# Performance work log

Measured on AMD Instinct MI355X. Metric: run time of the kernel, lower is better.

Reference implementation:

```python
import jax, jax.numpy as jnp
import numpy as np

A_, H_, D_, T_, B_ = 12, 6, 192, 80, 8
C_ = 192                      # GATv2 out_channels per head
N_ = B_ * A_                  # sequences
G_ = B_ * T_                  # graphs (one per frame)
E_ = A_ * (A_ - 1)            # 132 directed edges, no self loops
DH_ = D_ // H_


def _ln(x, g, b):
    m = jnp.mean(x, -1, keepdims=True)
    v = jnp.mean((x - m) ** 2, -1, keepdims=True)
    return (x - m) * jax.lax.rsqrt(v + 1e-5) * g + b


def _bn(x, g, b, m, v):  # eval-mode BatchNorm1d over the feature channel
    return (x - m) * jax.lax.rsqrt(v + 1e-5) * g + b


def _forward(state_feat, edge_attr, emb_table, laW1, lab1, bn1g, bn1b, bn1m, bn1v, laW2, lab2, bn2g, bn2b, bn2m, bn2v, laW3, lab3, bn3g, bn3b, bn3m, bn3v, ln1g, ln1b, qkvw, qkvb, outw, outb, ln2g, ln2b, fw1, fb1, fw2, fb2, gwl, gbl, gwr, gbr, gwe, gatt, gbias, ng, nb, padding_mask, agent_ids, edge_index):
    pl = emb_table[jnp.clip(agent_ids, 0)]                                   # [N,12]
    x = jnp.concatenate([state_feat, jnp.broadcast_to(pl[:, None, :], (N_, T_, 12))], -1)
    x = jax.nn.relu(_bn(x @ laW1 + lab1, bn1g, bn1b, bn1m, bn1v))
    x = jax.nn.relu(_bn(x @ laW2 + lab2, bn2g, bn2b, bn2m, bn2v))
    x = jax.nn.relu(_bn(x @ laW3 + lab3, bn3g, bn3b, bn3m, bn3v))
    x_initial = x
    # sinusoidal positional encoding (dropout off / eval)
    pos = jnp.arange(T_, dtype=jnp.float32)[:, None]
    div = jnp.exp(jnp.arange(0, D_, 2, dtype=jnp.float32) * (-np.log(10000.0) / D_))
    pe = jnp.zeros((T_, D_), jnp.float32).at[:, 0::2].set(jnp.sin(pos * div)).at[:, 1::2].set(jnp.cos(pos * div))
    x = x + pe
    causal = jnp.triu(jnp.full((T_, T_), -jnp.inf, jnp.float32), k=1)
    # --- static GAT edge structure (shared by every frame-graph) ---
    src, dst = edge_index[0], edge_index[1]
    onehot = (dst[None, :] == jnp.arange(A_)[:, None]).astype(jnp.float32)   # [A,E]
    cnt = onehot.sum(1)
    ea = edge_attr.reshape(G_, E_, 2)
    # PyG add_self_loops(fill_value='mean'): self-loop attr = mean of incoming-edge attrs
    loop_ea = jnp.einsum('ae,gef->gaf', onehot, ea) / cnt[None, :, None]     # [G,A,2]
    ea2 = jnp.concatenate([ea, loop_ea], axis=1).reshape(-1, 2)              # [G*(E+A),2]
    src2 = jnp.concatenate([src, jnp.arange(A_, dtype=src.dtype)])
    dst2 = jnp.concatenate([dst, jnp.arange(A_, dtype=dst.dtype)])
    off = (jnp.arange(G_, dtype=src.dtype) * A_)[:, None]
    sflat = (src2[None, :] + off).reshape(-1)                                # flattened batch-of-graphs
    dflat = (dst2[None, :] + off).reshape(-1)
    GA = G_ * A_
    for l in range(3):
        # --- causal temporal self-attention (pre-LN, eval: dropout off) ---
        xn = _ln(x, ln1g[l], ln1b[l])
        qkv = xn @ qkvw[l] + qkvb[l]
        q, k, v = jnp.split(qkv, 3, axis=-1)
        q = q.reshape(N_, T_, H_, DH_); k = k.reshape(N_, T_, H_, DH_); v = v.reshape(N_, T_, H_, DH_)
        s = jnp.einsum('nqhd,nkhd->nhqk', q, k) / np.sqrt(DH_) + causal
        s = jnp.where(padding_mask[:, None, None, :], -jnp.inf, s)
        p = jax.nn.softmax(s, axis=-1)
        o = jnp.einsum('nhqk,nkhd->nqhd', p, v).reshape(N_, T_, D_)
        x = x + (o @ outw[l] + outb[l])
        xn = _ln(x, ln2g[l], ln2b[l])
        x = x + (jax.nn.gelu(xn @ fw1[l] + fb1[l], approximate=False) @ fw2[l] + fb2[l])
        # --- framewise GATv2 (concat=False -> mean over heads) ---
        xn = _ln(x, ng[l], nb[l])
        xnodes = xn.reshape(B_, A_, T_, D_).transpose(0, 2, 1, 3).reshape(GA, D_)
        xl = (xnodes @ gwl[l] + gbl[l]).reshape(GA, H_, C_)
        xr = (xnodes @ gwr[l] + gbr[l]).reshape(GA, H_, C_)
        ef = (ea2 @ gwe[l]).reshape(-1, H_, C_)
        xls = xl[sflat]                                                      # gather source features
        msg = jax.nn.leaky_relu(xls + xr[dflat] + ef, 0.2)
        alpha = jnp.einsum('ehc,hc->eh', msg, gatt[l])
        amax = jax.lax.stop_gradient(jax.ops.segment_max(alpha, dflat, num_segments=GA))
        exs = jnp.exp(alpha - amax[dflat])
        den = jax.ops.segment_sum(exs, dflat, num_segments=GA)
        w = exs / den[dflat]                                                 # segment softmax over dst
        agg = jax.ops.segment_sum(w[:, :, None] * xls, dflat, num_segments=GA)
        xg = (agg.mean(axis=1) + gbias[l]).reshape(B_, T_, A_, D_).transpose(0, 2, 1, 3).reshape(N_, T_, D_)
        x = x + xg
    return (x_initial, x)


def setup_inputs():
    ks = iter(jax.random.split(jax.random.key(0), 60))
    def r(shape, s=0.05):
        return jax.random.normal(next(ks), shape, jnp.float32) * s
    pairs = np.array([(i, j) for i in range(A_) for j in range(A_) if i != j], dtype=np.int32)
    return dict(
        state_feat=jax.random.normal(next(ks), (N_, T_, 4), jnp.float32),
        padding_mask=jnp.zeros((N_, T_), bool),
        agent_ids=jax.random.randint(next(ks), (N_,), 0, 600, jnp.int32),
        edge_index=jnp.asarray(pairs.T),
        edge_attr=jax.random.normal(next(ks), (B_, T_, E_, 2), jnp.float32),
        emb_table=r((600, 12), 1.0),
        laW1=r((16, 64)), lab1=jnp.zeros((64,)),
        bn1g=jnp.ones((64,)), bn1b=jnp.zeros((64,)), bn1m=jnp.zeros((64,)), bn1v=jnp.ones((64,)),
        laW2=r((64, 256)), lab2=jnp.zeros((256,)),
        bn2g=jnp.ones((256,)), bn2b=jnp.zeros((256,)), bn2m=jnp.zeros((256,)), bn2v=jnp.ones((256,)),
        laW3=r((256, D_)), lab3=jnp.zeros((D_,)),
        bn3g=jnp.ones((D_,)), bn3b=jnp.zeros((D_,)), bn3m=jnp.zeros((D_,)), bn3v=jnp.ones((D_,)),
        ln1g=jnp.ones((3, D_)), ln1b=jnp.zeros((3, D_)),
        qkvw=r((3, D_, 3 * D_)), qkvb=jnp.zeros((3, 3 * D_)),
        outw=r((3, D_, D_)), outb=jnp.zeros((3, D_)),
        ln2g=jnp.ones((3, D_)), ln2b=jnp.zeros((3, D_)),
        fw1=r((3, D_, 4 * D_)), fb1=jnp.zeros((3, 4 * D_)),
        fw2=r((3, 4 * D_, D_)), fb2=jnp.zeros((3, D_)),
        gwl=r((3, D_, H_ * C_)), gbl=jnp.zeros((3, H_ * C_)),
        gwr=r((3, D_, H_ * C_)), gbr=jnp.zeros((3, H_ * C_)),
        gwe=r((3, 2, H_ * C_)),
        gatt=r((3, H_, C_)),
        gbias=jnp.zeros((3, D_)),
        ng=jnp.ones((3, D_)), nb=jnp.zeros((3, D_)),
    )


def reference(state_feat, padding_mask, agent_ids, edge_index, edge_attr, emb_table, laW1, lab1, bn1g, bn1b, bn1m, bn1v, laW2, lab2, bn2g, bn2b, bn2m, bn2v, laW3, lab3, bn3g, bn3b, bn3m, bn3v, ln1g, ln1b, qkvw, qkvb, outw, outb, ln2g, ln2b, fw1, fb1, fw2, fb2, gwl, gbl, gwr, gbr, gwe, gatt, gbias, ng, nb):
    return _forward(state_feat, edge_attr, emb_table, laW1, lab1, bn1g, bn1b, bn1m, bn1v, laW2, lab2, bn2g, bn2b, bn2m, bn2v, laW3, lab3, bn3g, bn3b, bn3m, bn3v, ln1g, ln1b, qkvw, qkvb, outw, outb, ln2g, ln2b, fw1, fb1, fw2, fb2, gwl, gbl, gwr, gbr, gwe, gatt, gbias, ng, nb, padding_mask, agent_ids, edge_index)
```

## Files before the change

kernel.cpp:

```cpp
#include <hip/hip_runtime.h>
#include <hip/hip_bf16.h>
#include <math.h>

#define A_   12
#define H_   6
#define N_   96
#define T_   80
#define G_   640
#define E_   132
#define E2_  144
#define ROWS_ 7680

typedef const __hip_bfloat16* bfp;
typedef __hip_bfloat16 bf16;
typedef __attribute__((ext_vector_type(8))) short short8;
typedef __attribute__((ext_vector_type(4))) short short4v;
typedef __attribute__((ext_vector_type(4))) float f32x4;

#define WB_QKV   0
#define WB_OUT   331776
#define WB_FW1   442368
#define WB_FW2   884736
#define WB_GAT   1327104
#define WB_W1    2654208
#define WB_W2    2655232
#define WB_W3T   2671616
#define WB_GWE   2720768
#define WB_GATT  2727680
#define WB_TOT   2731136
#define BB_QKV   0
#define BB_OUT   1728
#define BB_FW1   2304
#define BB_FW2   4608
#define BB_GAT   5184
#define BB_B1    12096
#define BB_B2    12160
#define BB_B3    12416
#define BB_TOT   12608

__device__ __forceinline__ float b2f(bf16 x){ return __bfloat162float(x); }
__device__ __forceinline__ float ldf(const void* p, size_t i, int f){
    return f ? __bfloat162float(((const bf16*)p)[i]) : ((const float*)p)[i];
}

__global__ void k_detect(const void* sf, int* flag)
{
    const unsigned short* u = (const unsigned short*)sf;
    int sane = 0;
    for (int i = 0; i < 64; i++){
        unsigned short v = u[2*i];
        int e = (v >> 7) & 0xFF;
        if (e == 0 || (e >= 100 && e <= 140)) sane++;
    }
    *flag = (sane >= 48) ? 1 : 0;
}

__global__ __launch_bounds__(256) void k_convert(
    const void* qkvw, const void* outw, const void* fw1, const void* fw2,
    const void* gwl, const void* gwr, const void* gwe, const void* gatt,
    const void* W1, const void* b1, const void* g1, const void* be1, const void* m1, const void* v1,
    const void* W2, const void* b2, const void* g2, const void* be2, const void* m2, const void* v2,
    const void* W3, const void* b3, const void* g3, const void* be3, const void* m3, const void* v3,
    const void* qkvb, const void* outb, const void* fb1, const void* fb2,
    const void* gbl, const void* gbr,
    const int* flagp, bf16* WB, float* BB)
{
    const int f = *flagp;
    size_t idx = (size_t)blockIdx.x*256 + threadIdx.x;
    if (idx < WB_TOT){
        float v;
        if (idx < WB_OUT){            size_t i=idx-WB_QKV; int l=i/110592; int r=i%110592; int n=r/192, k=r%192;
            v = ldf(qkvw, (size_t)l*110592 + (size_t)k*576 + n, f);
        } else if (idx < WB_FW1){     size_t i=idx-WB_OUT; int l=i/36864; int r=i%36864; int n=r/192, k=r%192;
            v = ldf(outw, (size_t)l*36864 + (size_t)k*192 + n, f);
        } else if (idx < WB_FW2){     size_t i=idx-WB_FW1; int l=i/147456; int r=i%147456; int n=r/192, k=r%192;
            v = ldf(fw1, (size_t)l*147456 + (size_t)k*768 + n, f);
        } else if (idx < WB_GAT){     size_t i=idx-WB_FW2; int l=i/147456; int r=i%147456; int n=r/768, k=r%768;
            v = ldf(fw2, (size_t)l*147456 + (size_t)k*192 + n, f);
        } else if (idx < WB_W1){      size_t i=idx-WB_GAT; int l=i/442368; int r=i%442368; int n=r/192, k=r%192;
            if (n < 1152) v = ldf(gwl, (size_t)l*221184 + (size_t)k*1152 + n, f);
            else          v = ldf(gwr, (size_t)l*221184 + (size_t)k*1152 + (n-1152), f);
        } else if (idx < WB_W2){      size_t i=idx-WB_W1; int o=i%64;
            float s = ldf(g1,o,f)*rsqrtf(ldf(v1,o,f)+1e-5f);
            v = ldf(W1, i, f) * s;
        } else if (idx < WB_W3T){     size_t i=idx-WB_W2; int o=i%256;
            float s = ldf(g2,o,f)*rsqrtf(ldf(v2,o,f)+1e-5f);
            v = ldf(W2, i, f) * s;
        } else if (idx < WB_GWE){     size_t i=idx-WB_W3T; int n=i/256, k=i%256;
            float s = ldf(g3,n,f)*rsqrtf(ldf(v3,n,f)+1e-5f);
            v = ldf(W3, (size_t)k*192 + n, f) * s;
        } else if (idx < WB_GATT){    size_t i=idx-WB_GWE;
            v = ldf(gwe, i, f);
        } else {                      size_t i=idx-WB_GATT;
            v = ldf(gatt, i, f);
        }
        WB[idx] = __float2bfloat16(v);
    } else if (idx < WB_TOT + BB_TOT){
        size_t j = idx - WB_TOT;
        float v;
        if (j < BB_OUT)        v = ldf(qkvb, j, f);
        else if (j < BB_FW1)   v = ldf(outb, j-BB_OUT, f);
        else if (j < BB_FW2)   v = ldf(fb1, j-BB_FW1, f);
        else if (j < BB_GAT)   v = ldf(fb2, j-BB_FW2, f);
        else if (j < BB_B1){   size_t i=j-BB_GAT; int l=i/2304; int o=i%2304;
            v = (o<1152) ? ldf(gbl, (size_t)l*1152+o, f) : ldf(gbr, (size_t)l*1152+o-1152, f);
        } else if (j < BB_B2){ int o=j-BB_B1;
            float s = ldf(g1,o,f)*rsqrtf(ldf(v1,o,f)+1e-5f);
            v = (ldf(b1,o,f)-ldf(m1,o,f))*s + ldf(be1,o,f);
        } else if (j < BB_B3){ int o=j-BB_B2;
            float s = ldf(g2,o,f)*rsqrtf(ldf(v2,o,f)+1e-5f);
            v = (ldf(b2,o,f)-ldf(m2,o,f))*s + ldf(be2,o,f);
        } else {               int o=j-BB_B3;
            float s = ldf(g3,o,f)*rsqrtf(ldf(v3,o,f)+1e-5f);
            v = (ldf(b3,o,f)-ldf(m3,o,f))*s + ldf(be3,o,f);
        }
        BB[j] = v;
    }
}

__global__ __launch_bounds__(256) void k_mlp_a(
    const void* sf, const int* ids, const void* emb, const int* flagp,
    const bf16* __restrict__ WB, const float* __restrict__ BB, bf16* h2g)
{
    __shared__ float in16[16][16];
    __shared__ float h1[16][64];
    const int f = *flagp;
    int tid = threadIdx.x;
    int row0 = blockIdx.x * 16;
    {
        int r = tid >> 4, i = tid & 15;
        int row = row0 + r;
        float v;
        if (i < 4) v = ldf(sf, (size_t)row*4 + i, f);
        else {
            int id = ids[row / T_]; if (id < 0) id = 0; if (id > 599) id = 599;
            v = ldf(emb, (size_t)id*12 + (i-4), f);
        }
        in16[r][i] = v;
    }
    __syncthreads();
    {
        int o = tid & 63, rg = tid >> 6;
        float acc[4];
        float bv = BB[BB_B1 + o];
        #pragma unroll
        for (int j=0;j<4;j++) acc[j] = bv;
        for (int i=0;i<16;i++){
            float w = b2f(WB[WB_W1 + i*64 + o]);
            #pragma unroll
            for (int j=0;j<4;j++) acc[j] += in16[rg*4+j][i]*w;
        }
        #pragma unroll
        for (int j=0;j<4;j++) h1[rg*4+j][o] = acc[j] > 0.f ? acc[j] : 0.f;
    }
    __syncthreads();
    {
        int o = tid;
        float acc[16];
        float bv = BB[BB_B2 + o];
        #pragma unroll
        for (int r=0;r<16;r++) acc[r] = bv;
        for (int i=0;i<64;i++){
            float w = b2f(WB[WB_W2 + i*256 + o]);
            #pragma unroll
            for (int r=0;r<16;r++) acc[r] += h1[r][i]*w;
        }
        for (int r=0;r<16;r++){
            float v = acc[r] > 0.f ? acc[r] : 0.f;
            h2g[(size_t)(row0+r)*256 + o] = __float2bfloat16(v);
        }
    }
}

__global__ __launch_bounds__(256) void k_mgemm(
    const bf16* __restrict__ A, const bf16* __restrict__ Wt, const float* __restrict__ bias,
    bf16* outh, float* outf, const float* __restrict__ res, void* out0, const int* flagp,
    int K, int N, int mode)
{
    __shared__ short As[64*200];
    __shared__ short Bs[64*200];
    int tid = threadIdx.x;
    int w = tid >> 6, lane = tid & 63, q = lane >> 4, li = lane & 15;
    int m0 = blockIdx.x * 64, n0 = blockIdx.y * 64;
    const int f = flagp ? *flagp : 0;
    f32x4 acc[4];
    #pragma unroll
    for (int nt=0;nt<4;nt++) acc[nt] = (f32x4){0.f,0.f,0.f,0.f};
    int nkc = (K + 191) / 192;
    for (int kc = 0; kc < nkc; kc++){
        int kcw = K - kc*192; if (kcw > 192) kcw = 192;
        int vr = kcw >> 3;
        const bf16* Ab = A  + (size_t)m0*K + kc*192;
        const bf16* Bb = Wt + (size_t)n0*K + kc*192;
        for (int idx = tid; idx < 64*vr; idx += 256){
            int r = idx / vr, kv = idx - r*vr;
            *(short8*)&As[r*200 + kv*8] = *(const short8*)&Ab[(size_t)r*K + kv*8];
        }
        for (int idx = tid; idx < 64*vr; idx += 256){
            int r = idx / vr, kv = idx - r*vr;
            *(short8*)&Bs[r*200 + kv*8] = *(const short8*)&Bb[(size_t)r*K + kv*8];
        }
        __syncthreads();
        int kkn = kcw >> 5;
        for (int kk = 0; kk < kkn; kk++){
            int ko = kk*32 + q*8;
            short8 a = *(short8*)&As[(w*16+li)*200 + ko];
            #pragma unroll
            for (int nt = 0; nt < 4; nt++){
                short8 b = *(short8*)&Bs[(nt*16+li)*200 + ko];
                acc[nt] = __builtin_amdgcn_mfma_f32_16x16x32_bf16(a, b, acc[nt], 0, 0, 0);
            }
        }
        __syncthreads();
    }
    int rb = m0 + w*16 + q*4;
    #pragma unroll
    for (int nt = 0; nt < 4; nt++){
        int col = n0 + nt*16 + li;
        float bv = bias[col];
        #pragma unroll
        for (int p = 0; p < 4; p++){
            int row = rb + p;
            float v = acc[nt][p] + bv;
            size_t idx = (size_t)row*N + col;
            if (mode == 0) outh[idx] = __float2bfloat16(v);
            else if (mode == 1) outh[idx] = __float2bfloat16(0.5f*v*(1.f + erff(v*0.70710678118654752f)));
            else if (mode == 2) outf[idx] = v + res[idx];
            else {
                float r2 = v > 0.f ? v : 0.f;
                if (f) ((bf16*)out0)[idx] = __float2bfloat16(r2);
                else   ((float*)out0)[idx] = r2;
                int t = row % T_;
                int i2 = col & ~1;
                float dv = expf((float)i2 * (-9.210340371976184f/192.f));
                float ang = (float)t * dv;
                outf[idx] = r2 + ((col & 1) ? cosf(ang) : sinf(ang));
            }
        }
    }
}

__global__ __launch_bounds__(256) void k_mgemm128(
    const bf16* __restrict__ A, const bf16* __restrict__ Wt, const float* __restrict__ bias,
    bf16* outh, int K, int N, int mode)
{
    __shared__ short As[128*104];
    __shared__ short Bs[64*104];
    int tid = threadIdx.x;
    int w = tid >> 6, lane = tid & 63, q = lane >> 4, li = lane & 15;
    int m0 = blockIdx.x * 128, n0 = blockIdx.y * 64;
    f32x4 acc[2][4];
    #pragma unroll
    for (int mt=0;mt<2;mt++)
        #pragma unroll
        for (int nt=0;nt<4;nt++) acc[mt][nt] = (f32x4){0.f,0.f,0.f,0.f};
    int nkc = K / 96;
    for (int kc = 0; kc < nkc; kc++){
        const bf16* Ab = A  + (size_t)m0*K + kc*96;
        const bf16* Bb = Wt + (size_t)n0*K + kc*96;
        for (int idx = tid; idx < 128*12; idx += 256){
            int r = idx / 12, kv = idx - r*12;
            *(short8*)&As[r*104 + kv*8] = *(const short8*)&Ab[(size_t)r*K + kv*8];
        }
        for (int idx = tid; idx < 64*12; idx += 256){
            int r = idx / 12, kv = idx - r*12;
            *(short8*)&Bs[r*104 + kv*8] = *(const short8*)&Bb[(size_t)r*K + kv*8];
        }
        __syncthreads();
        #pragma unroll
        for (int kk = 0; kk < 3; kk++){
            int ko = kk*32 + q*8;
            short8 b0 = *(short8*)&Bs[(0*16+li)*104 + ko];
            short8 b1 = *(short8*)&Bs[(1*16+li)*104 + ko];
            short8 b2 = *(short8*)&Bs[(2*16+li)*104 + ko];
            short8 b3 = *(short8*)&Bs[(3*16+li)*104 + ko];
            #pragma unroll
            for (int mt = 0; mt < 2; mt++){
                short8 a = *(short8*)&As[(w*32 + mt*16 + li)*104 + ko];
                acc[mt][0] = __builtin_amdgcn_mfma_f32_16x16x32_bf16(a, b0, acc[mt][0], 0, 0, 0);
                acc[mt][1] = __builtin_amdgcn_mfma_f32_16x16x32_bf16(a, b1, acc[mt][1], 0, 0, 0);
                acc[mt][2] = __builtin_amdgcn_mfma_f32_16x16x32_bf16(a, b2, acc[mt][2], 0, 0, 0);
                acc[mt][3] = __builtin_amdgcn_mfma_f32_16x16x32_bf16(a, b3, acc[mt][3], 0, 0, 0);
            }
        }
        __syncthreads();
    }
    #pragma unroll
    for (int mt = 0; mt < 2; mt++){
        int rb = m0 + w*32 + mt*16 + q*4;
        #pragma unroll
        for (int nt = 0; nt < 4; nt++){
            int col = n0 + nt*16 + li;
            float bv = bias[col];
            #pragma unroll
            for (int p = 0; p < 4; p++){
                float v = acc[mt][nt][p] + bv;
                size_t idx = (size_t)(rb+p)*N + col;
                if (mode == 0) outh[idx] = __float2bfloat16(v);
                else outh[idx] = __float2bfloat16(0.5f*v*(1.f + erff(v*0.70710678118654752f)));
            }
        }
    }
}

__global__ __launch_bounds__(256) void k_ln(const float* __restrict__ x, const void* g, const void* b,
                     size_t gOff, const int* flagp, bf16* out, int permute)
{
    const int f = *flagp;
    int tid = threadIdx.x;
    int row = blockIdx.x*4 + (tid>>6);
    int lane = tid & 63;
    const float* xr = x + (size_t)row*192;
    float v0 = xr[lane], v1 = xr[lane+64], v2 = xr[lane+128];
    float s = v0+v1+v2;
    float qq = v0*v0+v1*v1+v2*v2;
    #pragma unroll
    for (int off=32; off; off>>=1){ s += __shfl_xor(s, off); qq += __shfl_xor(qq, off); }
    float mean = s * (1.f/192.f);
    float var  = qq * (1.f/192.f) - mean*mean;
    float rs = rsqrtf(var + 1e-5f);
    int orow = row;
    if (permute){ int n = row/T_, t = row%T_; int bb = n/A_, a = n%A_; orow = (bb*T_+t)*A_ + a; }
    bf16* op = out + (size_t)orow*192;
    op[lane]     = __float2bfloat16((v0-mean)*rs*ldf(g,gOff+lane,f)     + ldf(b,gOff+lane,f));
    op[lane+64]  = __float2bfloat16((v1-mean)*rs*ldf(g,gOff+lane+64,f)  + ldf(b,gOff+lane+64,f));
    op[lane+128] = __float2bfloat16((v2-mean)*rs*ldf(g,gOff+lane+128,f) + ldf(b,gOff+lane+128,f));
}

__global__ __launch_bounds__(64) void k_attn(bfp qkv, bf16* attn_o)
{
    __shared__ float Ks[80][32];
    __shared__ float Vs[80][32];
    int bid = blockIdx.x;
    int qt = bid % 5;
    int nh = bid / 5;
    int n = nh / H_, h = nh % H_;
    int tid = threadIdx.x;
    for (int idx = tid; idx < 640; idx += 64){
        int r = idx >> 3, c4 = (idx & 7) << 2;
        const bf16* rp = qkv + (size_t)(n*T_+r)*576 + h*32 + c4;
        short4v kv = *(const short4v*)(rp + 192);
        short4v vv = *(const short4v*)(rp + 384);
        f32x4 kf, vf;
        #pragma unroll
        for (int e=0;e<4;e++){
            kf[e] = __uint_as_float(((unsigned)(unsigned short)kv[e])<<16);
            vf[e] = __uint_as_float(((unsigned)(unsigned short)vv[e])<<16);
        }
        *(f32x4*)&Ks[r][c4] = kf;
        *(f32x4*)&Vs[r][c4] = vf;
    }
    __syncthreads();
    int qi = tid & 15, p = tid >> 4;
    int q = qt*16 + qi;
    float qv[8];
    const bf16* qp = qkv + (size_t)(n*T_+q)*576 + h*32 + p*8;
    #pragma unroll
    for (int c=0;c<8;c++) qv[c] = b2f(qp[c]);
    float m = -1e30f, l = 0.f;
    float acc[8];
    #pragma unroll
    for (int c=0;c<8;c++) acc[c]=0.f;
    int jmax = qt*16 + 15;
    for (int j = 0; j <= jmax; j++){
        float s = 0.f;
        #pragma unroll
        for (int c=0;c<8;c++) s += qv[c]*Ks[j][p*8+c];
        s += __shfl_xor(s, 16);
        s += __shfl_xor(s, 32);
        s *= 0.17677669529663687f;
        if (j > q) s = -1e30f;
        float mn = fmaxf(m, s);
        float corr = expf(m - mn);
        float e = expf(s - mn);
        l = l*corr + e;
        #pragma unroll
        for (int c=0;c<8;c++) acc[c] = acc[c]*corr + e*Vs[j][p*8+c];
        m = mn;
    }
    float inv = 1.f/l;
    bf16* op = attn_o + (size_t)(n*T_+q)*192 + h*32 + p*8;
    #pragma unroll
    for (int c=0;c<8;c++) op[c] = __float2bfloat16(acc[c]*inv);
}

__global__ __launch_bounds__(192) void k_loopea(const int* __restrict__ eidx, const void* ea,
                                                const int* flagp, float* lea)
{
    __shared__ float s0[A_], s1[A_];
    __shared__ int cnt[A_];
    const int f = *flagp;
    int g = blockIdx.x;
    int tid = threadIdx.x;
    if (tid < A_){ s0[tid] = 0.f; s1[tid] = 0.f; cnt[tid] = 0; }
    __syncthreads();
    if (tid < E_){
        int d = eidx[E_ + tid];
        float a0 = ldf(ea, (size_t)(g*E_+tid)*2,   f);
        float a1 = ldf(ea, (size_t)(g*E_+tid)*2+1, f);
        atomicAdd(&s0[d], a0);
        atomicAdd(&s1[d], a1);
        atomicAdd(&cnt[d], 1);
    }
    __syncthreads();
    if (tid < A_){
        int c = cnt[tid] < 1 ? 1 : cnt[tid];
        lea[(g*A_+tid)*2]   = s0[tid]/(float)c;
        lea[(g*A_+tid)*2+1] = s1[tid]/(float)c;
    }
}

__global__ __launch_bounds__(256) void k_alpha(bfp xlr,
                        const float* __restrict__ lea, const void* ea,
                        const bf16* __restrict__ gweb, const bf16* __restrict__ gattb,
                        const int* flagp, float* alpha)
{
    const int f = *flagp;
    int wid = blockIdx.x*4 + (threadIdx.x>>6);
    int lane = threadIdx.x & 63;
    int g = wid / 144, ds = wid % 144;
    int d = ds / 12, s = ds % 12;
    float f0, f1;
    if (s == d){
        f0 = lea[(g*A_+s)*2]; f1 = lea[(g*A_+s)*2+1];
    } else {
        int el = s*11 + (d < s ? d : d-1);
        f0 = ldf(ea, (size_t)(g*E_+el)*2,   f);
        f1 = ldf(ea, (size_t)(g*E_+el)*2+1, f);
    }
    const bf16* xls = xlr + (size_t)(g*A_+s)*2304;
    const bf16* xrd = xlr + (size_t)(g*A_+d)*2304 + 1152;
    for (int h=0; h<H_; h++){
        float p = 0.f;
        #pragma unroll
        for (int c3=0;c3<3;c3++){
            int hc = h*192 + c3*64 + lane;
            float m = b2f(xls[hc]) + b2f(xrd[hc]) + f0*b2f(gweb[hc]) + f1*b2f(gweb[1152+hc]);
            m = m > 0.f ? m : 0.2f*m;
            p += m * b2f(gattb[hc]);
        }
        #pragma unroll
        for (int off=32; off; off>>=1) p += __shfl_xor(p, off);
        if (lane==0) alpha[(size_t)wid*H_ + h] = p;
    }
}

__global__ __launch_bounds__(192) void k_segagg(bfp xlr, const float* __restrict__ alpha,
                         const void* gbias, size_t gbOff, const int* flagp, float* xf)
{
    __shared__ float al[12][6];
    __shared__ float w[12][6];
    const int f = *flagp;
    int node = blockIdx.x;
    int gl = node / A_, a = node % A_;
    int tid = threadIdx.x;
    if (tid < 72) ((float*)al)[tid] = alpha[(size_t)node*72 + tid];
    __syncthreads();
    if (tid < 6){
        float m = -1e30f;
        #pragma unroll
        for (int s=0;s<12;s++) m = fmaxf(m, al[s][tid]);
        float den = 0.f;
        #pragma unroll
        for (int s=0;s<12;s++){ float ex = expf(al[s][tid]-m); w[s][tid] = ex; den += ex; }
        float inv = 1.f/den;
        #pragma unroll
        for (int s=0;s<12;s++) w[s][tid] *= inv;
    }
    __syncthreads();
    int c = tid;
    float acc = 0.f;
    for (int s=0;s<12;s++){
        const bf16* xp = xlr + (size_t)(gl*A_ + s)*2304 + c;
        #pragma unroll
        for (int h=0;h<6;h++) acc += w[s][h]*b2f(xp[h*192]);
    }
    int b = gl / T_, t = gl % T_;
    int xrow = (b*A_ + a)*T_ + t;
    xf[(size_t)xrow*192 + c] += acc*(1.f/6.f) + ldf(gbias, gbOff + c, f);
}

__global__ __launch_bounds__(256) void k_store(const float* __restrict__ xf, void* out, const int* flagp)
{
    const int f = *flagp;
    int i = blockIdx.x*256 + threadIdx.x;
    if (i < ROWS_*192){
        if (f) ((bf16*)out)[1474560 + i] = __float2bfloat16(xf[i]);
        else   ((float*)out)[1474560 + i] = xf[i];
    }
}

extern "C" void kernel_launch(void* const* d_in, const int* in_sizes, int n_in,
                              void* d_out, int out_size, void* d_ws, size_t ws_size,
                              hipStream_t stream)
{
    const void* sf   = d_in[0];
    const int* ids  = (const int*)d_in[2];
    const int* eidx = (const int*)d_in[3];
    const void* ea   = d_in[4];
    const void* emb  = d_in[5];
    const void *laW1=d_in[6],  *lab1=d_in[7];
    const void *bn1g=d_in[8],  *bn1b=d_in[9],  *bn1m=d_in[10], *bn1v=d_in[11];
    const void *laW2=d_in[12], *lab2=d_in[13];
    const void *bn2g=d_in[14], *bn2b=d_in[15], *bn2m=d_in[16], *bn2v=d_in[17];
    const void *laW3=d_in[18], *lab3=d_in[19];
    const void *bn3g=d_in[20], *bn3b=d_in[21], *bn3m=d_in[22], *bn3v=d_in[23];
    const void *ln1g=d_in[24], *ln1b=d_in[25];
    const void *qkvw=d_in[26], *qkvb=d_in[27];
    const void *outw=d_in[28], *outb=d_in[29];
    const void *ln2g=d_in[30], *ln2b=d_in[31];
    const void *fw1 =d_in[32], *fb1 =d_in[33];
    const void *fw2 =d_in[34], *fb2 =d_in[35];
    const void *gwl =d_in[36], *gbl =d_in[37];
    const void *gwr =d_in[38], *gbr =d_in[39];
    const void *gwe =d_in[40];
    const void *gatt=d_in[41];
    const void *gbias=d_in[42];
    const void *ng  =d_in[43], *nb  =d_in[44];

    float* ws = (float*)d_ws;
    float* xf  = ws;
    bf16*  xn  = (bf16*)(ws + 1474560);
    bf16*  qkv = (bf16*)(ws + 2211840);
    bf16*  ao  = (bf16*)(ws + 4423680);
    bf16*  hb  = (bf16*)(ws + 2211840);
    bf16*  h2  = (bf16*)(ws + 2211840);
    bf16*  xlr = (bf16*)(ws + 2211840);
    float* lea = ws + 11059200;
    int*  flag = (int*)(ws + 11074560);
    bf16*  WB  = (bf16*)(ws + 11074568);
    float* BB  = ws + 12440136;
    float* alp = ws + 12452744;
    (void)ws_size; (void)in_sizes; (void)n_in; (void)out_size;

    k_detect<<<1, 1, 0, stream>>>(sf, flag);
    k_convert<<<(WB_TOT+BB_TOT+255)/256, 256, 0, stream>>>(
        qkvw, outw, fw1, fw2, gwl, gwr, gwe, gatt,
        laW1, lab1, bn1g, bn1b, bn1m, bn1v,
        laW2, lab2, bn2g, bn2b, bn2m, bn2v,
        laW3, lab3, bn3g, bn3b, bn3m, bn3v,
        qkvb, outb, fb1, fb2, gbl, gbr, flag, WB, BB);
    k_mlp_a<<<ROWS_/16, 256, 0, stream>>>(sf, ids, emb, flag, WB, BB, h2);
    k_mgemm<<<dim3(ROWS_/64, 3), 256, 0, stream>>>(h2, WB + WB_W3T, BB + BB_B3,
        nullptr, xf, nullptr, d_out, flag, 256, 192, 3);
    k_loopea<<<G_, 192, 0, stream>>>(eidx, ea, flag, lea);

    for (int l=0; l<3; l++){
        k_ln<<<ROWS_/4, 256, 0, stream>>>(xf, ln1g, ln1b, (size_t)l*192, flag, xn, 0);
        k_mgemm128<<<dim3(ROWS_/128, 9), 256, 0, stream>>>(xn, WB + WB_QKV + (size_t)l*110592,
            BB + BB_QKV + l*576, qkv, 192, 576, 0);
        k_attn<<<N_*H_*5, 64, 0, stream>>>(qkv, ao);
        k_mgemm<<<dim3(ROWS_/64, 3), 256, 0, stream>>>(ao, WB + WB_OUT + (size_t)l*36864,
            BB + BB_OUT + l*192, nullptr, xf, xf, nullptr, nullptr, 192, 192, 2);
        k_ln<<<ROWS_/4, 256, 0, stream>>>(xf, ln2g, ln2b, (size_t)l*192, flag, xn, 0);
        k_mgemm128<<<dim3(ROWS_/128, 12), 256, 0, stream>>>(xn, WB + WB_FW1 + (size_t)l*147456,
            BB + BB_FW1 + l*768, hb, 192, 768, 1);
        k_mgemm<<<dim3(ROWS_/64, 3), 256, 0, stream>>>(hb, WB + WB_FW2 + (size_t)l*147456,
            BB + BB_FW2 + l*192, nullptr, xf, xf, nullptr, nullptr, 768, 192, 2);
        k_ln<<<ROWS_/4, 256, 0, stream>>>(xf, ng, nb, (size_t)l*192, flag, xn, 1);
        k_mgemm128<<<dim3(ROWS_/128, 36), 256, 0, stream>>>(xn, WB + WB_GAT + (size_t)l*442368,
            BB + BB_GAT + l*2304, xlr, 192, 2304, 0);
        k_alpha<<<G_*144/4, 256, 0, stream>>>(xlr, lea, ea,
            WB + WB_GWE + (size_t)l*2304, WB + WB_GATT + (size_t)l*1152, flag, alp);
        k_segagg<<<G_*A_, 192, 0, stream>>>(xlr, alp, gbias, (size_t)l*192, flag, xf);
    }
    k_store<<<(ROWS_*192+255)/256, 256, 0, stream>>>(xf, d_out, flag);
}
```

Before: 920.3 us.

## Use packed fp16 math with fdot2 for GATv2 attention logits

The GAT projection GEMM now writes xl/xr in fp16 instead of bf16, and the edge and attention weights are stored as fp16. The alpha kernel is rewritten to process two channels per operation with packed half arithmetic. LeakyReLU is expressed algebraically as 0.6*m + 0.4*|m| and accumulated with fdot2, with six contiguous channels per lane covering two heads per wave. This is meant to cut the ALU and load-instruction cost of the per-edge logit computation, but fp16 has less range than bf16 and the inner-loop products now run in half precision.

New measurement: 870.4 us. 5.4% less time.

```diff
diff --git a/kernel.cpp b/kernel.cpp
--- a/kernel.cpp
+++ b/kernel.cpp
@@ -16,6 +16,7 @@
 typedef __attribute__((ext_vector_type(8))) short short8;
 typedef __attribute__((ext_vector_type(4))) short short4v;
 typedef __attribute__((ext_vector_type(4))) float f32x4;
+typedef _Float16 h2 __attribute__((ext_vector_type(2)));
 
 #define WB_QKV   0
 #define WB_OUT   331776
@@ -68,7 +69,7 @@
     const int f = *flagp;
     size_t idx = (size_t)blockIdx.x*256 + threadIdx.x;
     if (idx < WB_TOT){
-        float v;
+        float v; int ishalf = 0;
         if (idx < WB_OUT){            size_t i=idx-WB_QKV; int l=i/110592; int r=i%110592; int n=r/192, k=r%192;
             v = ldf(qkvw, (size_t)l*110592 + (size_t)k*576 + n, f);
         } else if (idx < WB_FW1){     size_t i=idx-WB_OUT; int l=i/36864; int r=i%36864; int n=r/192, k=r%192;
@@ -90,11 +91,12 @@
             float s = ldf(g3,n,f)*rsqrtf(ldf(v3,n,f)+1e-5f);
             v = ldf(W3, (size_t)k*192 + n, f) * s;
         } else if (idx < WB_GATT){    size_t i=idx-WB_GWE;
-            v = ldf(gwe, i, f);
+            v = ldf(gwe, i, f); ishalf = 1;
         } else {                      size_t i=idx-WB_GATT;
-            v = ldf(gatt, i, f);
-        }
-        WB[idx] = __float2bfloat16(v);
+            v = ldf(gatt, i, f); ishalf = 1;
+        }
+        if (ishalf) ((_Float16*)WB)[idx] = (_Float16)v;
+        else        WB[idx] = __float2bfloat16(v);
     } else if (idx < WB_TOT + BB_TOT){
         size_t j = idx - WB_TOT;
         float v;
@@ -297,7 +299,8 @@
                 float v = acc[mt][nt][p] + bv;
                 size_t idx = (size_t)(rb+p)*N + col;
                 if (mode == 0) outh[idx] = __float2bfloat16(v);
-                else outh[idx] = __float2bfloat16(0.5f*v*(1.f + erff(v*0.70710678118654752f)));
+                else if (mode == 1) outh[idx] = __float2bfloat16(0.5f*v*(1.f + erff(v*0.70710678118654752f)));
+                else ((_Float16*)outh)[idx] = (_Float16)v;
             }
         }
     }
@@ -410,9 +413,9 @@
     }
 }
 
-__global__ __launch_bounds__(256) void k_alpha(bfp xlr,
+__global__ __launch_bounds__(256) void k_alpha(const _Float16* __restrict__ xlr,
                         const float* __restrict__ lea, const void* ea,
-                        const bf16* __restrict__ gweb, const bf16* __restrict__ gattb,
+                        const _Float16* __restrict__ gweh, const _Float16* __restrict__ gatth,
                         const int* flagp, float* alpha)
 {
     const int f = *flagp;
@@ -428,24 +431,40 @@
         f0 = ldf(ea, (size_t)(g*E_+el)*2,   f);
         f1 = ldf(ea, (size_t)(g*E_+el)*2+1, f);
     }
-    const bf16* xls = xlr + (size_t)(g*A_+s)*2304;
-    const bf16* xrd = xlr + (size_t)(g*A_+d)*2304 + 1152;
-    for (int h=0; h<H_; h++){
-        float p = 0.f;
-        #pragma unroll
-        for (int c3=0;c3<3;c3++){
-            int hc = h*192 + c3*64 + lane;
-            float m = b2f(xls[hc]) + b2f(xrd[hc]) + f0*b2f(gweb[hc]) + f1*b2f(gweb[1152+hc]);
-            m = m > 0.f ? m : 0.2f*m;
-            p += m * b2f(gattb[hc]);
-        }
-        #pragma unroll
-        for (int off=32; off; off>>=1) p += __shfl_xor(p, off);
-        if (lane==0) alpha[(size_t)wid*H_ + h] = p;
-    }
-}
-
-__global__ __launch_bounds__(192) void k_segagg(bfp xlr, const float* __restrict__ alpha,
+    h2 f0h = (h2){(_Float16)f0, (_Float16)f0};
+    h2 f1h = (h2){(_Float16)f1, (_Float16)f1};
+    const _Float16* xls = xlr + (size_t)(g*A_+s)*2304;
+    const _Float16* xrd = xlr + (size_t)(g*A_+d)*2304 + 1152;
+    int co = 6*lane;
+    #pragma unroll
+    for (int hg = 0; hg < 3; hg++){
+        int base = hg*384 + co;
+        float pA = 0.f, pB = 0.f;
+        #pragma unroll
+        for (int j = 0; j < 3; j++){
+            int o = base + 2*j;
+            h2 xl2 = *(const h2*)(xls + o);
+            h2 xr2 = *(const h2*)(xrd + o);
+            h2 g0  = *(const h2*)(gweh + o);
+            h2 g1  = *(const h2*)(gweh + 1152 + o);
+            h2 ga  = *(const h2*)(gatth + o);
+            h2 m = xl2 + xr2;
+            m = g0*f0h + m;
+            m = g1*f1h + m;
+            unsigned mu = __builtin_bit_cast(unsigned, m) & 0x7fff7fffu;
+            h2 am = __builtin_bit_cast(h2, mu);
+            pA = __builtin_amdgcn_fdot2(ga, m,  pA, false);
+            pB = __builtin_amdgcn_fdot2(ga, am, pB, false);
+        }
+        #pragma unroll
+        for (int off=1; off<32; off<<=1){ pA += __shfl_xor(pA, off); pB += __shfl_xor(pB, off); }
+        if ((lane & 31) == 0)
+            alpha[(size_t)wid*H_ + hg*2 + (lane>>5)] = 0.6f*pA + 0.4f*pB;
+    }
+}
+
+__global__ __launch_bounds__(192) void k_segagg(const _Float16* __restrict__ xlr,
+                         const float* __restrict__ alpha,
                          const void* gbias, size_t gbOff, const int* flagp, float* xf)
 {
     __shared__ float al[12][6];
@@ -471,9 +490,9 @@
     int c = tid;
     float acc = 0.f;
     for (int s=0;s<12;s++){
-        const bf16* xp = xlr + (size_t)(gl*A_ + s)*2304 + c;
-        #pragma unroll
-        for (int h=0;h<6;h++) acc += w[s][h]*b2f(xp[h*192]);
+        const _Float16* xp = xlr + (size_t)(gl*A_ + s)*2304 + c;
+        #pragma unroll
+        for (int h=0;h<6;h++) acc += w[s][h]*(float)xp[h*192];
     }
     int b = gl / T_, t = gl % T_;
     int xrow = (b*A_ + a)*T_ + t;
@@ -524,7 +543,7 @@
     bf16*  qkv = (bf16*)(ws + 2211840);
     bf16*  ao  = (bf16*)(ws + 4423680);
     bf16*  hb  = (bf16*)(ws + 2211840);
-    bf16*  h2  = (bf16*)(ws + 2211840);
+    bf16*  h2g = (bf16*)(ws + 2211840);
     bf16*  xlr = (bf16*)(ws + 2211840);
     float* lea = ws + 11059200;
     int*  flag = (int*)(ws + 11074560);
@@ -540,8 +559,8 @@
         laW2, lab2, bn2g, bn2b, bn2m, bn2v,
         laW3, lab3, bn3g, bn3b, bn3m, bn3v,
         qkvb, outb, fb1, fb2, gbl, gbr, flag, WB, BB);
-    k_mlp_a<<<ROWS_/16, 256, 0, stream>>>(sf, ids, emb, flag, WB, BB, h2);
-    k_mgemm<<<dim3(ROWS_/64, 3), 256, 0, stream>>>(h2, WB + WB_W3T, BB + BB_B3,
+    k_mlp_a<<<ROWS_/16, 256, 0, stream>>>(sf, ids, emb, flag, WB, BB, h2g);
+    k_mgemm<<<dim3(ROWS_/64, 3), 256, 0, stream>>>(h2g, WB + WB_W3T, BB + BB_B3,
         nullptr, xf, nullptr, d_out, flag, 256, 192, 3);
     k_loopea<<<G_, 192, 0, stream>>>(eidx, ea, flag, lea);
 
@@ -559,10 +578,11 @@
             BB + BB_FW2 + l*192, nullptr, xf, xf, nullptr, nullptr, 768, 192, 2);
         k_ln<<<ROWS_/4, 256, 0, stream>>>(xf, ng, nb, (size_t)l*192, flag, xn, 1);
         k_mgemm128<<<dim3(ROWS_/128, 36), 256, 0, stream>>>(xn, WB + WB_GAT + (size_t)l*442368,
-            BB + BB_GAT + l*2304, xlr, 192, 2304, 0);
-        k_alpha<<<G_*144/4, 256, 0, stream>>>(xlr, lea, ea,
-            WB + WB_GWE + (size_t)l*2304, WB + WB_GATT + (size_t)l*1152, flag, alp);
-        k_segagg<<<G_*A_, 192, 0, stream>>>(xlr, alp, gbias, (size_t)l*192, flag, xf);
+            BB + BB_GAT + l*2304, xlr, 192, 2304, 4);
+        k_alpha<<<G_*144/4, 256, 0, stream>>>((const _Float16*)xlr, lea, ea,
+            (const _Float16*)(WB + WB_GWE) + (size_t)l*2304,
+            (const _Float16*)(WB + WB_GATT) + (size_t)l*1152, flag, alp);
+        k_segagg<<<G_*A_, 192, 0, stream>>>((const _Float16*)xlr, alp, gbias, (size_t)l*192, flag, xf);
     }
     k_store<<<(ROWS_*192+255)/256, 256, 0, stream>>>(xf, d_out, flag);
 }
```
